# Optimization experiments

Hardware: AMD Instinct MI355X
Metric: run time of the kernel (lower is better)

The kernel has to match this reference:

```python
import jax, jax.numpy as jnp
import numpy as np

EPS = 1e-12  # tf.math.l2_normalize epsilon guard

def _l2_normalize(x, axis):
    sq = jnp.sum(x * x, axis=axis, keepdims=True)
    return x * jax.lax.rsqrt(jnp.maximum(sq, EPS))

def setup_inputs() -> dict:
    key = jax.random.key(0)
    k1, k2 = jax.random.split(key)
    a = jax.random.normal(k1, (16, 4096, 256), dtype=jnp.float32)
    b = jax.random.normal(k2, (16, 4096, 256), dtype=jnp.float32)
    return {"a": a, "b": b}

def reference(a, b):
    # Original: Dot(axes=[2,2], normalize=True) -> [B,N,N] cosine matrix,
    # then diag_part -> [B,N]. Diagonal entry (i) is cosine(a[:,i,:], b[:,i,:]),
    # so compute only the matching-row cosine similarity.
    a_hat = _l2_normalize(a, axis=2)
    b_hat = _l2_normalize(b, axis=2)
    return jnp.sum(a_hat * b_hat, axis=2)  # [B, N]
```

## Files before the change

kernel.cpp:

```cpp
#include <hip/hip_runtime.h>
#include <math.h>


#define EPS 1e-12f

__global__ __launch_bounds__(256) void cosine_rows_kernel(
    const float4* __restrict__ a4,
    const float4* __restrict__ b4,
    float* __restrict__ out,
    int nrows)
{
    const int wave = threadIdx.x >> 6;
    const int lane = threadIdx.x & 63;
    const int row  = (blockIdx.x << 2) + wave;
    if (row >= nrows) return;

    const int idx = row * 64 + lane;
    const float4 av = a4[idx];
    const float4 bv = b4[idx];

    float saa = av.x * av.x + av.y * av.y + av.z * av.z + av.w * av.w;
    float sbb = bv.x * bv.x + bv.y * bv.y + bv.z * bv.z + bv.w * bv.w;
    float sab = av.x * bv.x + av.y * bv.y + av.z * bv.z + av.w * bv.w;

    #pragma unroll
    for (int off = 32; off > 0; off >>= 1) {
        saa += __shfl_xor(saa, off, 64);
        sbb += __shfl_xor(sbb, off, 64);
        sab += __shfl_xor(sab, off, 64);
    }

    if (lane == 0) {
        const float denom = sqrtf(fmaxf(saa, EPS)) * sqrtf(fmaxf(sbb, EPS));
        out[row] = sab / denom;
    }
}

extern "C" void kernel_launch(void* const* d_in, const int* in_sizes, int n_in,
                              void* d_out, int out_size, void* d_ws, size_t ws_size,
                              hipStream_t stream) {
    const float* a = (const float*)d_in[0];
    const float* b = (const float*)d_in[1];
    float* out = (float*)d_out;

    const int nrows = out_size;
    const int blocks = (nrows + 3) / 4;

    cosine_rows_kernel<<<blocks, 256, 0, stream>>>(
        (const float4*)a, (const float4*)b, out, nrows);
}
```

Measured before the change: 137.6 us.

## Process eight rows per wave with grid-stride loop and deeper per-lane loads

Each wave now handles eight rows at once, with eight lanes per row, and each lane issues eight float4 loads per input before reducing. The shuffle reduction is cut to three steps within an 8-lane group. The grid is fixed at 1024 blocks with a grid-stride loop instead of one block per four rows. The aim is more memory-level parallelism per thread and less per-block launch and reduction overhead, at the cost of higher register use and a fixed grid that may underfill or imbalance the device. Each lane's eight loads for a row are strided 128 bytes apart, which may make coalescing less regular than before.

After: 143.5 us. 1.04x slower.

```diff
diff --git a/kernel.cpp b/kernel.cpp
--- a/kernel.cpp
+++ b/kernel.cpp
@@ -10,29 +10,53 @@
     float* __restrict__ out,
     int nrows)
 {
-    const int wave = threadIdx.x >> 6;
     const int lane = threadIdx.x & 63;
-    const int row  = (blockIdx.x << 2) + wave;
-    if (row >= nrows) return;
+    const int sl   = lane & 7;
+    const int sub  = lane >> 3;
+    const int waveGlobal = (blockIdx.x << 2) + (threadIdx.x >> 6);
+    const int totalWaves = gridDim.x << 2;
 
-    const int idx = row * 64 + lane;
-    const float4 av = a4[idx];
-    const float4 bv = b4[idx];
+    for (int rowbase = waveGlobal * 8; rowbase < nrows; rowbase += totalWaves * 8) {
+        const int row = rowbase + sub;
+        if (row >= nrows) break;
 
-    float saa = av.x * av.x + av.y * av.y + av.z * av.z + av.w * av.w;
-    float sbb = bv.x * bv.x + bv.y * bv.y + bv.z * bv.z + bv.w * bv.w;
-    float sab = av.x * bv.x + av.y * bv.y + av.z * bv.z + av.w * bv.w;
+        const float4* __restrict__ ap = a4 + row * 64 + sl;
+        const float4* __restrict__ bp = b4 + row * 64 + sl;
 
-    #pragma unroll
-    for (int off = 32; off > 0; off >>= 1) {
-        saa += __shfl_xor(saa, off, 64);
-        sbb += __shfl_xor(sbb, off, 64);
-        sab += __shfl_xor(sab, off, 64);
-    }
+        float4 av[8], bv[8];
+        #pragma unroll
+        for (int j = 0; j < 8; ++j) av[j] = ap[j * 8];
+        #pragma unroll
+        for (int j = 0; j < 8; ++j) bv[j] = bp[j * 8];
 
-    if (lane == 0) {
-        const float denom = sqrtf(fmaxf(saa, EPS)) * sqrtf(fmaxf(sbb, EPS));
-        out[row] = sab / denom;
+        float saa = 0.f, sbb = 0.f, sab = 0.f;
+        #pragma unroll
+        for (int j = 0; j < 8; ++j) {
+            saa = fmaf(av[j].x, av[j].x, saa);
+            saa = fmaf(av[j].y, av[j].y, saa);
+            saa = fmaf(av[j].z, av[j].z, saa);
+            saa = fmaf(av[j].w, av[j].w, saa);
+            sbb = fmaf(bv[j].x, bv[j].x, sbb);
+            sbb = fmaf(bv[j].y, bv[j].y, sbb);
+            sbb = fmaf(bv[j].z, bv[j].z, sbb);
+            sbb = fmaf(bv[j].w, bv[j].w, sbb);
+            sab = fmaf(av[j].x, bv[j].x, sab);
+            sab = fmaf(av[j].y, bv[j].y, sab);
+            sab = fmaf(av[j].z, bv[j].z, sab);
+            sab = fmaf(av[j].w, bv[j].w, sab);
+        }
+
+        #pragma unroll
+        for (int off = 1; off < 8; off <<= 1) {
+            saa += __shfl_xor(saa, off, 64);
+            sbb += __shfl_xor(sbb, off, 64);
+            sab += __shfl_xor(sab, off, 64);
+        }
+
+        if (sl == 0) {
+            const float denom = sqrtf(fmaxf(saa, EPS)) * sqrtf(fmaxf(sbb, EPS));
+            out[row] = sab / denom;
+        }
     }
 }
 
@@ -44,7 +68,7 @@
     float* out = (float*)d_out;
 
     const int nrows = out_size;
-    const int blocks = (nrows + 3) / 4;
+    const int blocks = 1024;
 
     cosine_rows_kernel<<<blocks, 256, 0, stream>>>(
         (const float4*)a, (const float4*)b, out, nrows);
```

## Use grid-stride waves processing four rows each with nontemporal loads

Applied to the files above, without the earlier changes.

Replaces one-row-per-wave launch with a fixed grid of 2048 blocks where each wave handles four consecutive rows per iteration, issuing eight vector loads up front for more memory-level parallelism. Loads use nontemporal hints to avoid polluting caches on streaming data. Risks: assumes nrows is a multiple of 4 (true for 65536) and the fixed grid size may under- or over-subscribe the device.

New measurement: 136.8 us. No clear change (-0.6%).

```diff
diff --git a/kernel.cpp b/kernel.cpp
--- a/kernel.cpp
+++ b/kernel.cpp
@@ -4,35 +4,55 @@
 
 #define EPS 1e-12f
 
+typedef float f4 __attribute__((ext_vector_type(4)));
+
 __global__ __launch_bounds__(256) void cosine_rows_kernel(
-    const float4* __restrict__ a4,
-    const float4* __restrict__ b4,
+    const f4* __restrict__ a4,
+    const f4* __restrict__ b4,
     float* __restrict__ out,
     int nrows)
 {
-    const int wave = threadIdx.x >> 6;
     const int lane = threadIdx.x & 63;
-    const int row  = (blockIdx.x << 2) + wave;
-    if (row >= nrows) return;
+    const int wid  = (blockIdx.x << 2) + (threadIdx.x >> 6);
+    const int nw   = gridDim.x << 2;
 
-    const int idx = row * 64 + lane;
-    const float4 av = a4[idx];
-    const float4 bv = b4[idx];
+    for (int base = wid * 4; base < nrows; base += nw * 4) {
+        const int i0 = (base + 0) * 64 + lane;
+        const int i1 = (base + 1) * 64 + lane;
+        const int i2 = (base + 2) * 64 + lane;
+        const int i3 = (base + 3) * 64 + lane;
+        f4 av0 = __builtin_nontemporal_load(&a4[i0]);
+        f4 av1 = __builtin_nontemporal_load(&a4[i1]);
+        f4 av2 = __builtin_nontemporal_load(&a4[i2]);
+        f4 av3 = __builtin_nontemporal_load(&a4[i3]);
+        f4 bv0 = __builtin_nontemporal_load(&b4[i0]);
+        f4 bv1 = __builtin_nontemporal_load(&b4[i1]);
+        f4 bv2 = __builtin_nontemporal_load(&b4[i2]);
+        f4 bv3 = __builtin_nontemporal_load(&b4[i3]);
 
-    float saa = av.x * av.x + av.y * av.y + av.z * av.z + av.w * av.w;
-    float sbb = bv.x * bv.x + bv.y * bv.y + bv.z * bv.z + bv.w * bv.w;
-    float sab = av.x * bv.x + av.y * bv.y + av.z * bv.z + av.w * bv.w;
+        f4 avs[4] = {av0, av1, av2, av3};
+        f4 bvs[4] = {bv0, bv1, bv2, bv3};
 
-    #pragma unroll
-    for (int off = 32; off > 0; off >>= 1) {
-        saa += __shfl_xor(saa, off, 64);
-        sbb += __shfl_xor(sbb, off, 64);
-        sab += __shfl_xor(sab, off, 64);
-    }
+        #pragma unroll
+        for (int r = 0; r < 4; ++r) {
+            const f4 av = avs[r];
+            const f4 bv = bvs[r];
+            float saa = av.x * av.x + av.y * av.y + av.z * av.z + av.w * av.w;
+            float sbb = bv.x * bv.x + bv.y * bv.y + bv.z * bv.z + bv.w * bv.w;
+            float sab = av.x * bv.x + av.y * bv.y + av.z * bv.z + av.w * bv.w;
 
-    if (lane == 0) {
-        const float denom = sqrtf(fmaxf(saa, EPS)) * sqrtf(fmaxf(sbb, EPS));
-        out[row] = sab / denom;
+            #pragma unroll
+            for (int off = 32; off > 0; off >>= 1) {
+                saa += __shfl_xor(saa, off, 64);
+                sbb += __shfl_xor(sbb, off, 64);
+                sab += __shfl_xor(sab, off, 64);
+            }
+
+            if (lane == 0) {
+                const float denom = sqrtf(fmaxf(saa, EPS)) * sqrtf(fmaxf(sbb, EPS));
+                out[base + r] = sab / denom;
+            }
+        }
     }
 }
 
@@ -44,8 +64,8 @@
     float* out = (float*)d_out;
 
     const int nrows = out_size;
-    const int blocks = (nrows + 3) / 4;
+    const int blocks = 2048;
 
     cosine_rows_kernel<<<blocks, 256, 0, stream>>>(
-        (const float4*)a, (const float4*)b, out, nrows);
+        (const f4*)a, (const f4*)b, out, nrows);
 }
```

## Double-buffer row loads into LDS via async global_load_lds in persistent grid

Applied to the files above, without the earlier changes.

Replaces the one-row-per-wave kernel with a persistent grid of 1024 blocks in which each wave processes four rows per iteration. It double-buffers the next group's rows into LDS with global_load_lds DMA and s_waitcnt, so memory loads overlap compute. The reduction becomes a 16-lane shuffle per row rather than a 64-lane one. The aim is to keep more bytes in flight on a memory-bound stream, at the cost of LDS round trips, a fixed grid size, and hand-written waitcnt assumptions.

Result: slower. 142.8 us (+3.8%).

```diff
diff --git a/kernel.cpp b/kernel.cpp
--- a/kernel.cpp
+++ b/kernel.cpp
@@ -4,35 +4,82 @@
 
 #define EPS 1e-12f
 
-__global__ __launch_bounds__(256) void cosine_rows_kernel(
-    const float4* __restrict__ a4,
-    const float4* __restrict__ b4,
+typedef float f4 __attribute__((ext_vector_type(4)));
+
+__device__ __forceinline__ void dma16(const f4* g, f4* l) {
+    __builtin_amdgcn_global_load_lds(
+        (__attribute__((address_space(1))) void*)g,
+        (__attribute__((address_space(3))) void*)l,
+        16, 0, 0);
+}
+
+__global__ __launch_bounds__(128) void cosine_rows_kernel(
+    const f4* __restrict__ a4,
+    const f4* __restrict__ b4,
     float* __restrict__ out,
     int nrows)
 {
-    const int wave = threadIdx.x >> 6;
-    const int lane = threadIdx.x & 63;
-    const int row  = (blockIdx.x << 2) + wave;
-    if (row >= nrows) return;
+    __shared__ f4 lds[2][2][2][256];
 
-    const int idx = row * 64 + lane;
-    const float4 av = a4[idx];
-    const float4 bv = b4[idx];
+    const int w      = threadIdx.x >> 6;
+    const int lane   = threadIdx.x & 63;
+    const int W      = blockIdx.x * 2 + w;
+    const int stride = gridDim.x * 2 * 4;
 
-    float saa = av.x * av.x + av.y * av.y + av.z * av.z + av.w * av.w;
-    float sbb = bv.x * bv.x + bv.y * bv.y + bv.z * bv.z + bv.w * bv.w;
-    float sab = av.x * bv.x + av.y * bv.y + av.z * bv.z + av.w * bv.w;
-
-    #pragma unroll
-    for (int off = 32; off > 0; off >>= 1) {
-        saa += __shfl_xor(saa, off, 64);
-        sbb += __shfl_xor(sbb, off, 64);
-        sab += __shfl_xor(sab, off, 64);
+    int base = W * 4;
+    if (base < nrows) {
+        #pragma unroll
+        for (int r = 0; r < 4; ++r)
+            dma16(&a4[(base + r) * 64 + lane], &lds[w][0][0][r * 64]);
+        #pragma unroll
+        for (int r = 0; r < 4; ++r)
+            dma16(&b4[(base + r) * 64 + lane], &lds[w][0][1][r * 64]);
     }
 
-    if (lane == 0) {
-        const float denom = sqrtf(fmaxf(saa, EPS)) * sqrtf(fmaxf(sbb, EPS));
-        out[row] = sab / denom;
+    int buf = 0;
+    for (; base < nrows; base += stride, buf ^= 1) {
+        const int nxt = base + stride;
+        if (nxt < nrows) {
+            #pragma unroll
+            for (int r = 0; r < 4; ++r)
+                dma16(&a4[(nxt + r) * 64 + lane], &lds[w][buf ^ 1][0][r * 64]);
+            #pragma unroll
+            for (int r = 0; r < 4; ++r)
+                dma16(&b4[(nxt + r) * 64 + lane], &lds[w][buf ^ 1][1][r * 64]);
+            asm volatile("s_waitcnt vmcnt(8)" ::: "memory");
+        } else {
+            asm volatile("s_waitcnt vmcnt(0)" ::: "memory");
+        }
+
+        const int g  = lane >> 4;
+        const int sl = lane & 15;
+        const f4* __restrict__ ar = &lds[w][buf][0][g * 64];
+        const f4* __restrict__ br = &lds[w][buf][1][g * 64];
+
+        float saa = 0.f, sbb = 0.f, sab = 0.f;
+        #pragma unroll
+        for (int j = 0; j < 4; ++j) {
+            const f4 av = ar[sl + 16 * j];
+            const f4 bv = br[sl + 16 * j];
+            saa = fmaf(av.x, av.x, saa); saa = fmaf(av.y, av.y, saa);
+            saa = fmaf(av.z, av.z, saa); saa = fmaf(av.w, av.w, saa);
+            sbb = fmaf(bv.x, bv.x, sbb); sbb = fmaf(bv.y, bv.y, sbb);
+            sbb = fmaf(bv.z, bv.z, sbb); sbb = fmaf(bv.w, bv.w, sbb);
+            sab = fmaf(av.x, bv.x, sab); sab = fmaf(av.y, bv.y, sab);
+            sab = fmaf(av.z, bv.z, sab); sab = fmaf(av.w, bv.w, sab);
+        }
+
+        #pragma unroll
+        for (int off = 1; off < 16; off <<= 1) {
+            saa += __shfl_xor(saa, off, 64);
+            sbb += __shfl_xor(sbb, off, 64);
+            sab += __shfl_xor(sab, off, 64);
+        }
+
+        if (sl == 0) {
+            const float denom = sqrtf(fmaxf(saa, EPS)) * sqrtf(fmaxf(sbb, EPS));
+            out[base + g] = sab / denom;
+        }
     }
 }
 
@@ -44,8 +91,8 @@
     float* out = (float*)d_out;
 
     const int nrows = out_size;
-    const int blocks = (nrows + 3) / 4;
+    const int blocks = 1024;
 
-    cosine_rows_kernel<<<blocks, 256, 0, stream>>>(
-        (const float4*)a, (const float4*)b, out, nrows);
+    cosine_rows_kernel<<<blocks, 128, 0, stream>>>(
+        (const f4*)a, (const f4*)b, out, nrows);
 }
```
